# Optimization experiments

Hardware: AMD Instinct MI355X
Metric: run time of the kernel (lower is better)

The kernel has to match this reference:

```python
import jax, jax.numpy as jnp
import numpy as np

B, N, K, C_IN, M, C_OUT = 2, 20000, 16, 128, 9, 128


def setup_inputs() -> dict:
    key = jax.random.key(0)
    k1, k2, k3, k4, k5, k6 = jax.random.split(key, 6)
    x = jax.random.normal(k1, (B, N, C_IN), dtype=jnp.float32)
    # 0 == "no neighbor" (maps to the prepended zero row); valid ids are 1..N
    adj = jax.random.randint(k2, (N, K), 0, N, dtype=jnp.int32)
    W = jax.random.uniform(k3, (M, C_OUT, C_IN), jnp.float32, -0.05, 0.05)
    b = jax.random.uniform(k4, (C_OUT,), jnp.float32, -0.05, 0.05)
    u = jax.random.uniform(k5, (M, C_IN), jnp.float32, -0.05, 0.05)
    c = jax.random.uniform(k6, (M,), jnp.float32, -0.05, 0.05)
    return {"x": x, "adj": adj, "W": W, "b": b, "u": u, "c": c}


def reference(x, adj, W, b, u, c):
    Bb, Nn, Cin = x.shape
    # prepend zero row so adj==0 gathers zeros (padding neighbor)
    xp = jnp.concatenate([jnp.zeros((Bb, 1, Cin), x.dtype), x], axis=1)
    patches = xp[:, adj]                      # [B, N, K, C] neighbor features
    # pseudo-coordinate differences -> soft assignment over M kernels
    diff = x[:, :, None, :] - patches          # [B, N, K, C]
    logits = jnp.einsum('bnkc,mc->bnkm', diff, u) + c
    q = jax.nn.softmax(logits, axis=-1)        # softmax over M (last axis)
    # inverse neighbor count (0 where the node has no neighbors)
    deg = jnp.count_nonzero(adj, axis=1).astype(x.dtype)        # [N]
    deg_inv = jnp.where(deg > 0, 1.0 / jnp.maximum(deg, 1.0), 0.0)
    # out[b,n,o] = deg_inv[n] * sum_{k,m} q[b,n,k,m] * (W[m] @ x_nbr)[o]
    msg = jnp.einsum('bnkm,moc,bnkc->bno', q, W, patches)        # [B, N, O]
    return msg * deg_inv[None, :, None] + b
```

## Files before the change

kernel.cpp:

```cpp
#include <hip/hip_runtime.h>
#include <hip/hip_bf16.h>

#define NB 2
#define NN 20000
#define NKN 16
#define NC 128
#define NM 9
#define NO 128
#define NR (NB*NN)
#define KK (NM*NC)
#define NKC (KK/32)
#define NPB 32
#define YS 12
#define QS (NKN*12+4)
#define YB (NR/64)

typedef short bf16x8 __attribute__((ext_vector_type(8)));
typedef float f32x4 __attribute__((ext_vector_type(4)));
typedef float f32x2 __attribute__((ext_vector_type(2)));
typedef unsigned short u16x8 __attribute__((ext_vector_type(8)));

__device__ inline f32x2 bfpair(unsigned int w) {
    union { unsigned int u; float f; } lo, hi;
    lo.u = w << 16; hi.u = w & 0xFFFF0000u;
    return (f32x2){lo.f, hi.f};
}

__global__ __launch_bounds__(256) void prep_kernel(const float* __restrict__ x,
                                                   const float* __restrict__ u,
                                                   const float* __restrict__ W,
                                                   float* __restrict__ y,
                                                   __hip_bfloat16* __restrict__ xb,
                                                   __hip_bfloat16* __restrict__ Wg,
                                                   int use_xb) {
    int tid = threadIdx.x;
    if (blockIdx.x < YB) {
        int wave = tid >> 6, lane = tid & 63;
        int lr = lane & 15, quad = lane >> 4;
        int node0 = blockIdx.x * 64 + wave * 16;
        long xbase = (long)(node0 + lr) * NC;

        bf16x8 afr[4];
        #pragma unroll
        for (int kc = 0; kc < 4; kc++) {
            const float* px = x + xbase + kc * 32 + quad * 8;
            float4 a0 = *(const float4*)px;
            float4 a1 = *(const float4*)(px + 4);
            union { bf16x8 v; unsigned short s[8]; __hip_bfloat16 h[8]; } af;
            af.h[0] = __float2bfloat16(a0.x); af.h[1] = __float2bfloat16(a0.y);
            af.h[2] = __float2bfloat16(a0.z); af.h[3] = __float2bfloat16(a0.w);
            af.h[4] = __float2bfloat16(a1.x); af.h[5] = __float2bfloat16(a1.y);
            af.h[6] = __float2bfloat16(a1.z); af.h[7] = __float2bfloat16(a1.w);
            afr[kc] = af.v;
            if (use_xb)
                *(u16x8*)((unsigned short*)xb + xbase + kc * 32 + quad * 8) =
                    *(u16x8*)&af.v;
        }
        int cs = (lr < NM) ? lr : 0;
        float fz = (lr < NM) ? 1.f : 0.f;
        f32x4 acc = (f32x4){0.f, 0.f, 0.f, 0.f};
        #pragma unroll
        for (int kc = 0; kc < 4; kc++) {
            const float* pu = u + cs * NC + kc * 32 + quad * 8;
            float4 b0 = *(const float4*)pu;
            float4 b1 = *(const float4*)(pu + 4);
            union { bf16x8 v; __hip_bfloat16 h[8]; } bf;
            bf.h[0] = __float2bfloat16(b0.x * fz); bf.h[1] = __float2bfloat16(b0.y * fz);
            bf.h[2] = __float2bfloat16(b0.z * fz); bf.h[3] = __float2bfloat16(b0.w * fz);
            bf.h[4] = __float2bfloat16(b1.x * fz); bf.h[5] = __float2bfloat16(b1.y * fz);
            bf.h[6] = __float2bfloat16(b1.z * fz); bf.h[7] = __float2bfloat16(b1.w * fz);
            acc = __builtin_amdgcn_mfma_f32_16x16x32_bf16(afr[kc], bf.v, acc, 0, 0, 0);
        }
        if (lr < NM) {
            #pragma unroll
            for (int r = 0; r < 4; r++)
                y[(long)(node0 + quad * 4 + r) * YS + lr] = acc[r];
        }
    } else {
        int t = (blockIdx.x - YB) * 256 + tid;
        int kk = t >> 7;
        int o = t & 127;
        int m = kk >> 7;
        int c = kk & 127;
        float v = W[m * 16384 + o * 128 + c];
        Wg[((kk >> 5) * 128 + o) * 32 + (kk & 31)] = __float2bfloat16(v);
    }
}

template<bool BF16G>
__global__ __launch_bounds__(512, 4) void fused_kernel(const float* __restrict__ x,
                                                       const __hip_bfloat16* __restrict__ xb,
                                                       const int* __restrict__ adj,
                                                       const float* __restrict__ y,
                                                       const float* __restrict__ cv,
                                                       const __hip_bfloat16* __restrict__ Wg,
                                                       const float* __restrict__ bv,
                                                       float* __restrict__ out) {
    __shared__ __align__(16) short s_S[NPB * KK];
    float* s_q = (float*)s_S;

    int tid = threadIdx.x;
    int node0 = blockIdx.x * NPB;
    int b = node0 / NN;
    int n0 = node0 - b * NN;
    int ln = tid >> 4, k = tid & 15;

    const int* arow = adj + (n0 + ln) * NKN;
    int a = arow[k];
    int4 r0 = *(const int4*)arow;
    int4 r1 = *(const int4*)(arow + 4);
    int4 r2 = *(const int4*)(arow + 8);
    int4 r3 = *(const int4*)(arow + 12);

    const float* yn = y + (long)(node0 + ln) * YS;
    const float* ya = y + (long)(b * NN + ((a > 0) ? a - 1 : 0)) * YS;
    float4 yn0 = *(const float4*)yn;
    float4 yn1 = *(const float4*)(yn + 4);
    float  yn8 = yn[8];
    float4 ya0 = *(const float4*)ya;
    float4 ya1 = *(const float4*)(ya + 4);
    float  ya8 = ya[8];

    int idx[NKN]; int d = 0;
    #define PUT(J, V) { int aa = (V); d += (aa > 0); idx[J] = (aa > 0) ? aa - 1 : 0; }
    PUT(0, r0.x)  PUT(1, r0.y)  PUT(2, r0.z)  PUT(3, r0.w)
    PUT(4, r1.x)  PUT(5, r1.y)  PUT(6, r1.z)  PUT(7, r1.w)
    PUT(8, r2.x)  PUT(9, r2.y)  PUT(10, r2.z) PUT(11, r2.w)
    PUT(12, r3.x) PUT(13, r3.y) PUT(14, r3.z) PUT(15, r3.w)
    #undef PUT
    float di = (d > 0) ? 1.f / (float)d : 0.f;

    int c8 = k << 3;
    uint4 pw0[8];
    if (BF16G) {
        #pragma unroll
        for (int j = 0; j < 8; j++)
            pw0[j] = *(const uint4*)((const unsigned short*)xb +
                                     (long)(b * NN + idx[j]) * NC + c8);
    }

    {
        float sel = (a > 0) ? 1.f : 0.f;
        float l[NM];
        l[0] = yn0.x - sel * ya0.x + cv[0];
        l[1] = yn0.y - sel * ya0.y + cv[1];
        l[2] = yn0.z - sel * ya0.z + cv[2];
        l[3] = yn0.w - sel * ya0.w + cv[3];
        l[4] = yn1.x - sel * ya1.x + cv[4];
        l[5] = yn1.y - sel * ya1.y + cv[5];
        l[6] = yn1.z - sel * ya1.z + cv[6];
        l[7] = yn1.w - sel * ya1.w + cv[7];
        l[8] = yn8   - sel * ya8   + cv[8];
        float mx = l[0];
        #pragma unroll
        for (int m = 1; m < NM; m++) mx = fmaxf(mx, l[m]);
        float e[NM]; float sum = 0.f;
        #pragma unroll
        for (int m = 0; m < NM; m++) { e[m] = expf(l[m] - mx); sum += e[m]; }
        float qs = (a > 0) ? (1.f / sum) : 0.f;
        #pragma unroll
        for (int m = 0; m < NM; m++) s_q[ln * QS + k * 12 + m] = e[m] * qs;
    }
    asm volatile("s_waitcnt lgkmcnt(0)" ::: "memory");
    __builtin_amdgcn_sched_barrier(0);

    f32x2 s2[NM][4];
    #pragma unroll
    for (int m = 0; m < NM; m++)
        #pragma unroll
        for (int j = 0; j < 4; j++) s2[m][j] = (f32x2){0.f, 0.f};

    #define ACC_ALL(P0, P1, P2, P3, KK2) {                                    \
        const float* qr = &s_q[ln * QS + (KK2) * 12];                         \
        float4 qa = *(const float4*)qr;                                       \
        float4 qb = *(const float4*)(qr + 4);                                 \
        float  q8 = qr[8];                                                    \
        f32x2 qq;                                                             \
        qq=(f32x2){qa.x,qa.x}; s2[0][0]+=qq*P0; s2[0][1]+=qq*P1; s2[0][2]+=qq*P2; s2[0][3]+=qq*P3; \
        qq=(f32x2){qa.y,qa.y}; s2[1][0]+=qq*P0; s2[1][1]+=qq*P1; s2[1][2]+=qq*P2; s2[1][3]+=qq*P3; \
        qq=(f32x2){qa.z,qa.z}; s2[2][0]+=qq*P0; s2[2][1]+=qq*P1; s2[2][2]+=qq*P2; s2[2][3]+=qq*P3; \
        qq=(f32x2){qa.w,qa.w}; s2[3][0]+=qq*P0; s2[3][1]+=qq*P1; s2[3][2]+=qq*P2; s2[3][3]+=qq*P3; \
        qq=(f32x2){qb.x,qb.x}; s2[4][0]+=qq*P0; s2[4][1]+=qq*P1; s2[4][2]+=qq*P2; s2[4][3]+=qq*P3; \
        qq=(f32x2){qb.y,qb.y}; s2[5][0]+=qq*P0; s2[5][1]+=qq*P1; s2[5][2]+=qq*P2; s2[5][3]+=qq*P3; \
        qq=(f32x2){qb.z,qb.z}; s2[6][0]+=qq*P0; s2[6][1]+=qq*P1; s2[6][2]+=qq*P2; s2[6][3]+=qq*P3; \
        qq=(f32x2){qb.w,qb.w}; s2[7][0]+=qq*P0; s2[7][1]+=qq*P1; s2[7][2]+=qq*P2; s2[7][3]+=qq*P3; \
        qq=(f32x2){q8,q8};     s2[8][0]+=qq*P0; s2[8][1]+=qq*P1; s2[8][2]+=qq*P2; s2[8][3]+=qq*P3; }

    if (BF16G) {
        uint4 pw1[8];
        #pragma unroll
        for (int j = 0; j < 8; j++)
            pw1[j] = *(const uint4*)((const unsigned short*)xb +
                                     (long)(b * NN + idx[8 + j]) * NC + c8);
        #pragma unroll
        for (int j = 0; j < 8; j++) {
            f32x2 p0 = bfpair(pw0[j].x), p1 = bfpair(pw0[j].y);
            f32x2 p2 = bfpair(pw0[j].z), p3 = bfpair(pw0[j].w);
            ACC_ALL(p0, p1, p2, p3, j)
        }
        #pragma unroll
        for (int j = 0; j < 8; j++) {
            f32x2 p0 = bfpair(pw1[j].x), p1 = bfpair(pw1[j].y);
            f32x2 p2 = bfpair(pw1[j].z), p3 = bfpair(pw1[j].w);
            ACC_ALL(p0, p1, p2, p3, 8 + j)
        }
    } else {
        #pragma unroll
        for (int g = 0; g < NKN / 4; g++) {
            float4 fa[4], fb[4];
            #pragma unroll
            for (int j = 0; j < 4; j++) {
                const float* px = x + (long)(b * NN + idx[g * 4 + j]) * NC + c8;
                fa[j] = *(const float4*)px;
                fb[j] = *(const float4*)(px + 4);
            }
            #pragma unroll
            for (int j = 0; j < 4; j++) {
                f32x2 p0 = (f32x2){fa[j].x, fa[j].y}, p1 = (f32x2){fa[j].z, fa[j].w};
                f32x2 p2 = (f32x2){fb[j].x, fb[j].y}, p3 = (f32x2){fb[j].z, fb[j].w};
                ACC_ALL(p0, p1, p2, p3, g * 4 + j)
            }
        }
    }
    #undef ACC_ALL
    __syncthreads();

    #pragma unroll
    for (int m = 0; m < NM; m++) {
        u16x8 ov;
        #pragma unroll
        for (int j = 0; j < 4; j++) {
            union { unsigned short h; __hip_bfloat16 bb; } c0, c1;
            c0.bb = __float2bfloat16(s2[m][j][0] * di);
            c1.bb = __float2bfloat16(s2[m][j][1] * di);
            ov[j * 2]     = c0.h;
            ov[j * 2 + 1] = c1.h;
        }
        int g = m * 16 + k;
        int gs = g ^ (ln & 7);
        *(u16x8*)(&s_S[ln * KK + gs * 8]) = ov;
    }
    __syncthreads();

    int wave = tid >> 6;
    int lane = tid & 63;
    int lr = lane & 15;
    int quad = lane >> 4;
    const short* wg = reinterpret_cast<const short*>(Wg);
    f32x4 acc0 = (f32x4){0.f, 0.f, 0.f, 0.f};
    f32x4 acc1 = (f32x4){0.f, 0.f, 0.f, 0.f};

    #pragma unroll 9
    for (int kc = 0; kc < NKC; kc++) {
        int g = kc * 4 + quad;
        int gs = g ^ (lr & 7);
        bf16x8 bfrag = *(const bf16x8*)(wg + ((kc * 128) + wave * 16 + lr) * 32 + quad * 8);
        bf16x8 a0 = *(const bf16x8*)(&s_S[lr * KK + gs * 8]);
        bf16x8 a1 = *(const bf16x8*)(&s_S[(16 + lr) * KK + gs * 8]);
        acc0 = __builtin_amdgcn_mfma_f32_16x16x32_bf16(a0, bfrag, acc0, 0, 0, 0);
        acc1 = __builtin_amdgcn_mfma_f32_16x16x32_bf16(a1, bfrag, acc1, 0, 0, 0);
    }

    int col = wave * 16 + lr;
    float bb = bv[col];
    int rbase = node0 + quad * 4;
    #pragma unroll
    for (int r = 0; r < 4; r++) {
        out[(long)(rbase + r) * NO + col]      = acc0[r] + bb;
        out[(long)(rbase + 16 + r) * NO + col] = acc1[r] + bb;
    }
}

extern "C" void kernel_launch(void* const* d_in, const int* in_sizes, int n_in,
                              void* d_out, int out_size, void* d_ws, size_t ws_size,
                              hipStream_t stream) {
    const float* x   = (const float*)d_in[0];
    const int*   adj = (const int*)  d_in[1];
    const float* W   = (const float*)d_in[2];
    const float* bv  = (const float*)d_in[3];
    const float* u   = (const float*)d_in[4];
    const float* cv  = (const float*)d_in[5];
    float* out = (float*)d_out;

    char* ws = (char*)d_ws;
    float* y = (float*)ws;
    __hip_bfloat16* Wg = (__hip_bfloat16*)(ws + 1920000);
    __hip_bfloat16* xb = (__hip_bfloat16*)(ws + 2214912);
    bool use_xb = (ws_size >= (size_t)12454912);

    prep_kernel<<<YB + 576, 256, 0, stream>>>(x, u, W, y, use_xb ? xb : nullptr, Wg,
                                              use_xb ? 1 : 0);
    if (use_xb)
        fused_kernel<true><<<NR / NPB, 512, 0, stream>>>(x, xb, adj, y, cv, Wg, bv, out);
    else
        fused_kernel<false><<<NR / NPB, 512, 0, stream>>>(x, xb, adj, y, cv, Wg, bv, out);
}
```

Baseline: 134.3 us.

## Halve nodes per block and split channels across 32 threads per node

Each block now handles 16 nodes instead of 32, with 32 threads per node each gathering 4 channels instead of 16 threads gathering 8. This halves per-thread accumulator registers and shared memory, doubles the grid, and aims for higher occupancy and more latency hiding on the random neighbor gathers. The degree normalization is folded into the softmax weights and expf becomes __expf. In exchange, each MFMA wave now covers one 16-row tile, so every block reloads the full weight matrix for half as many rows, doubling weight traffic.

```diff
diff --git a/kernel.cpp b/kernel.cpp
--- a/kernel.cpp
+++ b/kernel.cpp
@@ -10,15 +10,17 @@
 #define NR (NB*NN)
 #define KK (NM*NC)
 #define NKC (KK/32)
-#define NPB 32
+#define NPB 16
 #define YS 12
 #define QS (NKN*12+4)
 #define YB (NR/64)
 
 typedef short bf16x8 __attribute__((ext_vector_type(8)));
+typedef short bf16x4 __attribute__((ext_vector_type(4)));
 typedef float f32x4 __attribute__((ext_vector_type(4)));
 typedef float f32x2 __attribute__((ext_vector_type(2)));
 typedef unsigned short u16x8 __attribute__((ext_vector_type(8)));
+typedef unsigned int u32x2 __attribute__((ext_vector_type(2)));
 
 __device__ inline f32x2 bfpair(unsigned int w) {
     union { unsigned int u; float f; } lo, hi;
@@ -103,14 +105,21 @@
     int node0 = blockIdx.x * NPB;
     int b = node0 / NN;
     int n0 = node0 - b * NN;
-    int ln = tid >> 4, k = tid & 15;
+    int ln = tid >> 5, cg = tid & 31;
+    int k16 = cg & 15;
 
     const int* arow = adj + (n0 + ln) * NKN;
-    int a = arow[k];
+    int a = arow[k16];
     int4 r0 = *(const int4*)arow;
     int4 r1 = *(const int4*)(arow + 4);
     int4 r2 = *(const int4*)(arow + 8);
     int4 r3 = *(const int4*)(arow + 12);
+
+    int d = (r0.x > 0) + (r0.y > 0) + (r0.z > 0) + (r0.w > 0)
+          + (r1.x > 0) + (r1.y > 0) + (r1.z > 0) + (r1.w > 0)
+          + (r2.x > 0) + (r2.y > 0) + (r2.z > 0) + (r2.w > 0)
+          + (r3.x > 0) + (r3.y > 0) + (r3.z > 0) + (r3.w > 0);
+    float di = (d > 0) ? 1.f / (float)d : 0.f;
 
     const float* yn = y + (long)(node0 + ln) * YS;
     const float* ya = y + (long)(b * NN + ((a > 0) ? a - 1 : 0)) * YS;
@@ -121,22 +130,19 @@
     float4 ya1 = *(const float4*)(ya + 4);
     float  ya8 = ya[8];
 
-    int idx[NKN]; int d = 0;
-    #define PUT(J, V) { int aa = (V); d += (aa > 0); idx[J] = (aa > 0) ? aa - 1 : 0; }
-    PUT(0, r0.x)  PUT(1, r0.y)  PUT(2, r0.z)  PUT(3, r0.w)
-    PUT(4, r1.x)  PUT(5, r1.y)  PUT(6, r1.z)  PUT(7, r1.w)
-    PUT(8, r2.x)  PUT(9, r2.y)  PUT(10, r2.z) PUT(11, r2.w)
-    PUT(12, r3.x) PUT(13, r3.y) PUT(14, r3.z) PUT(15, r3.w)
-    #undef PUT
-    float di = (d > 0) ? 1.f / (float)d : 0.f;
-
-    int c8 = k << 3;
-    uint4 pw0[8];
+    int c4 = cg << 2;
+    u32x2 pw0[8];
+    #define ROW(AA) ((long)(b * NN + (((AA) > 0) ? (AA) - 1 : 0)))
     if (BF16G) {
-        #pragma unroll
-        for (int j = 0; j < 8; j++)
-            pw0[j] = *(const uint4*)((const unsigned short*)xb +
-                                     (long)(b * NN + idx[j]) * NC + c8);
+        const unsigned short* xbs = (const unsigned short*)xb;
+        pw0[0] = *(const u32x2*)(xbs + ROW(r0.x) * NC + c4);
+        pw0[1] = *(const u32x2*)(xbs + ROW(r0.y) * NC + c4);
+        pw0[2] = *(const u32x2*)(xbs + ROW(r0.z) * NC + c4);
+        pw0[3] = *(const u32x2*)(xbs + ROW(r0.w) * NC + c4);
+        pw0[4] = *(const u32x2*)(xbs + ROW(r1.x) * NC + c4);
+        pw0[5] = *(const u32x2*)(xbs + ROW(r1.y) * NC + c4);
+        pw0[6] = *(const u32x2*)(xbs + ROW(r1.z) * NC + c4);
+        pw0[7] = *(const u32x2*)(xbs + ROW(r1.w) * NC + c4);
     }
 
     {
@@ -156,89 +162,87 @@
         for (int m = 1; m < NM; m++) mx = fmaxf(mx, l[m]);
         float e[NM]; float sum = 0.f;
         #pragma unroll
-        for (int m = 0; m < NM; m++) { e[m] = expf(l[m] - mx); sum += e[m]; }
-        float qs = (a > 0) ? (1.f / sum) : 0.f;
-        #pragma unroll
-        for (int m = 0; m < NM; m++) s_q[ln * QS + k * 12 + m] = e[m] * qs;
+        for (int m = 0; m < NM; m++) { e[m] = __expf(l[m] - mx); sum += e[m]; }
+        float qs = ((a > 0) ? (1.f / sum) : 0.f) * di;
+        #pragma unroll
+        for (int m = 0; m < NM; m++) s_q[ln * QS + k16 * 12 + m] = e[m] * qs;
     }
     asm volatile("s_waitcnt lgkmcnt(0)" ::: "memory");
     __builtin_amdgcn_sched_barrier(0);
 
-    f32x2 s2[NM][4];
+    f32x2 s2[NM][2];
     #pragma unroll
-    for (int m = 0; m < NM; m++)
-        #pragma unroll
-        for (int j = 0; j < 4; j++) s2[m][j] = (f32x2){0.f, 0.f};
-
-    #define ACC_ALL(P0, P1, P2, P3, KK2) {                                    \
+    for (int m = 0; m < NM; m++) {
+        s2[m][0] = (f32x2){0.f, 0.f};
+        s2[m][1] = (f32x2){0.f, 0.f};
+    }
+
+    #define ACC4(P0, P1, KK2) {                                               \
         const float* qr = &s_q[ln * QS + (KK2) * 12];                         \
         float4 qa = *(const float4*)qr;                                       \
         float4 qb = *(const float4*)(qr + 4);                                 \
         float  q8 = qr[8];                                                    \
         f32x2 qq;                                                             \
-        qq=(f32x2){qa.x,qa.x}; s2[0][0]+=qq*P0; s2[0][1]+=qq*P1; s2[0][2]+=qq*P2; s2[0][3]+=qq*P3; \
-        qq=(f32x2){qa.y,qa.y}; s2[1][0]+=qq*P0; s2[1][1]+=qq*P1; s2[1][2]+=qq*P2; s2[1][3]+=qq*P3; \
-        qq=(f32x2){qa.z,qa.z}; s2[2][0]+=qq*P0; s2[2][1]+=qq*P1; s2[2][2]+=qq*P2; s2[2][3]+=qq*P3; \
-        qq=(f32x2){qa.w,qa.w}; s2[3][0]+=qq*P0; s2[3][1]+=qq*P1; s2[3][2]+=qq*P2; s2[3][3]+=qq*P3; \
-        qq=(f32x2){qb.x,qb.x}; s2[4][0]+=qq*P0; s2[4][1]+=qq*P1; s2[4][2]+=qq*P2; s2[4][3]+=qq*P3; \
-        qq=(f32x2){qb.y,qb.y}; s2[5][0]+=qq*P0; s2[5][1]+=qq*P1; s2[5][2]+=qq*P2; s2[5][3]+=qq*P3; \
-        qq=(f32x2){qb.z,qb.z}; s2[6][0]+=qq*P0; s2[6][1]+=qq*P1; s2[6][2]+=qq*P2; s2[6][3]+=qq*P3; \
-        qq=(f32x2){qb.w,qb.w}; s2[7][0]+=qq*P0; s2[7][1]+=qq*P1; s2[7][2]+=qq*P2; s2[7][3]+=qq*P3; \
-        qq=(f32x2){q8,q8};     s2[8][0]+=qq*P0; s2[8][1]+=qq*P1; s2[8][2]+=qq*P2; s2[8][3]+=qq*P3; }
+        qq=(f32x2){qa.x,qa.x}; s2[0][0]+=qq*P0; s2[0][1]+=qq*P1;              \
+        qq=(f32x2){qa.y,qa.y}; s2[1][0]+=qq*P0; s2[1][1]+=qq*P1;              \
+        qq=(f32x2){qa.z,qa.z}; s2[2][0]+=qq*P0; s2[2][1]+=qq*P1;              \
+        qq=(f32x2){qa.w,qa.w}; s2[3][0]+=qq*P0; s2[3][1]+=qq*P1;              \
+        qq=(f32x2){qb.x,qb.x}; s2[4][0]+=qq*P0; s2[4][1]+=qq*P1;              \
+        qq=(f32x2){qb.y,qb.y}; s2[5][0]+=qq*P0; s2[5][1]+=qq*P1;              \
+        qq=(f32x2){qb.z,qb.z}; s2[6][0]+=qq*P0; s2[6][1]+=qq*P1;              \
+        qq=(f32x2){qb.w,qb.w}; s2[7][0]+=qq*P0; s2[7][1]+=qq*P1;              \
+        qq=(f32x2){q8,q8};     s2[8][0]+=qq*P0; s2[8][1]+=qq*P1; }
 
     if (BF16G) {
-        uint4 pw1[8];
-        #pragma unroll
-        for (int j = 0; j < 8; j++)
-            pw1[j] = *(const uint4*)((const unsigned short*)xb +
-                                     (long)(b * NN + idx[8 + j]) * NC + c8);
+        const unsigned short* xbs = (const unsigned short*)xb;
+        u32x2 pw1[8];
+        pw1[0] = *(const u32x2*)(xbs + ROW(r2.x) * NC + c4);
+        pw1[1] = *(const u32x2*)(xbs + ROW(r2.y) * NC + c4);
+        pw1[2] = *(const u32x2*)(xbs + ROW(r2.z) * NC + c4);
+        pw1[3] = *(const u32x2*)(xbs + ROW(r2.w) * NC + c4);
+        pw1[4] = *(const u32x2*)(xbs + ROW(r3.x) * NC + c4);
+        pw1[5] = *(const u32x2*)(xbs + ROW(r3.y) * NC + c4);
+        pw1[6] = *(const u32x2*)(xbs + ROW(r3.z) * NC + c4);
+        pw1[7] = *(const u32x2*)(xbs + ROW(r3.w) * NC + c4);
         #pragma unroll
         for (int j = 0; j < 8; j++) {
-            f32x2 p0 = bfpair(pw0[j].x), p1 = bfpair(pw0[j].y);
-            f32x2 p2 = bfpair(pw0[j].z), p3 = bfpair(pw0[j].w);
-            ACC_ALL(p0, p1, p2, p3, j)
+            f32x2 p0 = bfpair(pw0[j][0]), p1 = bfpair(pw0[j][1]);
+            ACC4(p0, p1, j)
         }
         #pragma unroll
         for (int j = 0; j < 8; j++) {
-            f32x2 p0 = bfpair(pw1[j].x), p1 = bfpair(pw1[j].y);
-            f32x2 p2 = bfpair(pw1[j].z), p3 = bfpair(pw1[j].w);
-            ACC_ALL(p0, p1, p2, p3, 8 + j)
+            f32x2 p0 = bfpair(pw1[j][0]), p1 = bfpair(pw1[j][1]);
+            ACC4(p0, p1, 8 + j)
         }
     } else {
-        #pragma unroll
-        for (int g = 0; g < NKN / 4; g++) {
-            float4 fa[4], fb[4];
-            #pragma unroll
-            for (int j = 0; j < 4; j++) {
-                const float* px = x + (long)(b * NN + idx[g * 4 + j]) * NC + c8;
-                fa[j] = *(const float4*)px;
-                fb[j] = *(const float4*)(px + 4);
-            }
-            #pragma unroll
-            for (int j = 0; j < 4; j++) {
-                f32x2 p0 = (f32x2){fa[j].x, fa[j].y}, p1 = (f32x2){fa[j].z, fa[j].w};
-                f32x2 p2 = (f32x2){fb[j].x, fb[j].y}, p3 = (f32x2){fb[j].z, fb[j].w};
-                ACC_ALL(p0, p1, p2, p3, g * 4 + j)
-            }
-        }
-    }
-    #undef ACC_ALL
+        int idx[NKN];
+        idx[0]=ROW(r0.x); idx[1]=ROW(r0.y); idx[2]=ROW(r0.z); idx[3]=ROW(r0.w);
+        idx[4]=ROW(r1.x); idx[5]=ROW(r1.y); idx[6]=ROW(r1.z); idx[7]=ROW(r1.w);
+        idx[8]=ROW(r2.x); idx[9]=ROW(r2.y); idx[10]=ROW(r2.z); idx[11]=ROW(r2.w);
+        idx[12]=ROW(r3.x); idx[13]=ROW(r3.y); idx[14]=ROW(r3.z); idx[15]=ROW(r3.w);
+        #pragma unroll
+        for (int j = 0; j < NKN; j++) {
+            float4 fa = *(const float4*)(x + (long)idx[j] * NC + c4);
+            f32x2 p0 = (f32x2){fa.x, fa.y}, p1 = (f32x2){fa.z, fa.w};
+            ACC4(p0, p1, j)
+        }
+    }
+    #undef ACC4
+    #undef ROW
     __syncthreads();
 
     #pragma unroll
     for (int m = 0; m < NM; m++) {
-        u16x8 ov;
-        #pragma unroll
-        for (int j = 0; j < 4; j++) {
-            union { unsigned short h; __hip_bfloat16 bb; } c0, c1;
-            c0.bb = __float2bfloat16(s2[m][j][0] * di);
-            c1.bb = __float2bfloat16(s2[m][j][1] * di);
-            ov[j * 2]     = c0.h;
-            ov[j * 2 + 1] = c1.h;
-        }
-        int g = m * 16 + k;
+        union { bf16x4 v; unsigned short h[4]; } ov;
+        union { unsigned short h; __hip_bfloat16 bb; } c0, c1, c2, c3;
+        c0.bb = __float2bfloat16(s2[m][0][0]);
+        c1.bb = __float2bfloat16(s2[m][0][1]);
+        c2.bb = __float2bfloat16(s2[m][1][0]);
+        c3.bb = __float2bfloat16(s2[m][1][1]);
+        ov.h[0] = c0.h; ov.h[1] = c1.h; ov.h[2] = c2.h; ov.h[3] = c3.h;
+        int g = m * 16 + (cg >> 1);
         int gs = g ^ (ln & 7);
-        *(u16x8*)(&s_S[ln * KK + gs * 8]) = ov;
+        *(bf16x4*)(&s_S[ln * KK + gs * 8 + (cg & 1) * 4]) = ov.v;
     }
     __syncthreads();
 
@@ -248,7 +252,6 @@
     int quad = lane >> 4;
     const short* wg = reinterpret_cast<const short*>(Wg);
     f32x4 acc0 = (f32x4){0.f, 0.f, 0.f, 0.f};
-    f32x4 acc1 = (f32x4){0.f, 0.f, 0.f, 0.f};
 
     #pragma unroll 9
     for (int kc = 0; kc < NKC; kc++) {
@@ -256,19 +259,15 @@
         int gs = g ^ (lr & 7);
         bf16x8 bfrag = *(const bf16x8*)(wg + ((kc * 128) + wave * 16 + lr) * 32 + quad * 8);
         bf16x8 a0 = *(const bf16x8*)(&s_S[lr * KK + gs * 8]);
-        bf16x8 a1 = *(const bf16x8*)(&s_S[(16 + lr) * KK + gs * 8]);
         acc0 = __builtin_amdgcn_mfma_f32_16x16x32_bf16(a0, bfrag, acc0, 0, 0, 0);
-        acc1 = __builtin_amdgcn_mfma_f32_16x16x32_bf16(a1, bfrag, acc1, 0, 0, 0);
     }
 
     int col = wave * 16 + lr;
     float bb = bv[col];
     int rbase = node0 + quad * 4;
     #pragma unroll
-    for (int r = 0; r < 4; r++) {
-        out[(long)(rbase + r) * NO + col]      = acc0[r] + bb;
-        out[(long)(rbase + 16 + r) * NO + col] = acc1[r] + bb;
-    }
+    for (int r = 0; r < 4; r++)
+        out[(long)(rbase + r) * NO + col] = acc0[r] + bb;
 }
 
 extern "C" void kernel_launch(void* const* d_in, const int* in_sizes, int n_in,
```

After: 151.9 us. 13.1% more time.
